# Optimization experiments

Measured on AMD Instinct MI355X. Metric: run time of the kernel, lower is better.

## Reference

```python
import jax, jax.numpy as jnp
import numpy as np

M_TIME = 64      # signal model output length (time points)
N_DICT = 20000   # dictionary entries
B_VOX = 8192     # voxels / batch


def setup_inputs() -> dict:
    key = jax.random.key(0)
    k = jax.random.split(key, 6)
    input_real = jax.random.normal(k[0], (M_TIME, B_VOX), jnp.float32)
    input_imag = jax.random.normal(k[1], (M_TIME, B_VOX), jnp.float32)
    # raw dictionary signals, then normalize columns as append() does
    yr = jax.random.normal(k[2], (M_TIME, N_DICT), jnp.float32)
    yi = jax.random.normal(k[3], (M_TIME, N_DICT), jnp.float32)
    norm = jnp.sqrt(jnp.sum(yr * yr + yi * yi, axis=0))  # (N,)
    inverse_norm_y = 1.0 / norm
    y_real = yr * inverse_norm_y
    y_imag = yi * inverse_norm_y
    x_t1 = jax.random.uniform(k[4], (N_DICT,), jnp.float32, 0.1, 3.0)
    x_t2 = jax.random.uniform(k[5], (N_DICT,), jnp.float32, 0.01, 0.5)
    return {
        'input_real': input_real, 'input_imag': input_imag,
        'y_real': y_real, 'y_imag': y_imag,
        'inverse_norm_y': inverse_norm_y, 'x_t1': x_t1, 'x_t2': x_t2,
    }


def reference(input_real, input_imag, y_real, y_imag, inverse_norm_y, x_t1, x_t2):
    # |<y_n, s_b>|^2 for complex y and complex input, via 4 real GEMMs (as in the
    # original module): sim[n, b]
    sim = (jnp.einsum('mb,mn->nb', input_real, y_real) ** 2
           + jnp.einsum('mb,mn->nb', input_real, y_imag) ** 2
           + jnp.einsum('mb,mn->nb', input_imag, y_real) ** 2
           + jnp.einsum('mb,mn->nb', input_imag, y_imag) ** 2)
    idx = jnp.argmax(sim, axis=0)  # (B,)
    # scale = sum_m conj(y[:, idx]) * input * inverse_norm_y[idx]
    yr = y_real[:, idx]   # (M, B)
    yi = y_imag[:, idx]   # (M, B)
    inv = inverse_norm_y[idx]  # (B,)
    scale_r = jnp.sum(yr * input_real + yi * input_imag, axis=0) * inv
    scale_i = jnp.sum(yr * input_imag - yi * input_real, axis=0) * inv
    # returns (scale, t1, t2) with complex scale split into real/imag, stacked (4, B)
    return jnp.stack([scale_r, scale_i, x_t1[idx], x_t2[idx]])
```

## Files before the change

kernel.cpp:

```cpp
#include <hip/hip_runtime.h>
#include <hip/hip_bf16.h>
#include <stdint.h>

#define M_TIME 64
#define N_DICT 20000
#define B_VOX  8192

#define NTILES 313

typedef _Float16 v8h __attribute__((ext_vector_type(8)));
typedef float    v4f __attribute__((ext_vector_type(4)));
typedef float    v2f __attribute__((ext_vector_type(2)));

__device__ __forceinline__ unsigned long long u64max(unsigned long long a, unsigned long long b) { return a > b ? a : b; }
__device__ __forceinline__ unsigned umin32(unsigned a, unsigned b) { return a < b ? a : b; }
__device__ __forceinline__ unsigned umax32(unsigned a, unsigned b) { return a > b ? a : b; }
__device__ __forceinline__ unsigned umed3(unsigned a, unsigned b, unsigned c) {
    unsigned d;
    asm("v_med3_u32 %0, %1, %2, %3" : "=v"(d) : "v"(a), "v"(b), "v"(c));
    return d;
}

__global__ __launch_bounds__(256) void split_y(
    const float* __restrict__ yr, const float* __restrict__ yi,
    v8h* __restrict__ yp)
{
    const int u = blockIdx.x * 256 + threadIdx.x;
    const int n_l = u & 63;
    const int j   = (u >> 6) & 7;
    const int T   = (u >> 9) % NTILES;
    const int arr = u / (NTILES * 512);
    if (arr > 1) return;
    const float* P = arr ? yi : yr;
    const int n_g = T * 64 + n_l;
    v8h V;
#pragma unroll
    for (int c = 0; c < 8; ++c) {
        float v = 0.f;
        if (n_g < N_DICT) v = P[(j * 8 + c) * N_DICT + n_g];
        V[c] = (_Float16)v;
    }
    const int fr = (arr * 2 + (j >> 2)) * 4 + (j & 3);
    yp[((size_t)T * 16 + fr) * 64 + n_l] = V;
}

__global__ __launch_bounds__(256, 2) void gemm_pre(
    const float* __restrict__ ir, const float* __restrict__ ii,
    const v8h* __restrict__ yp,
    unsigned* __restrict__ cand, int tpc, int slots)
{
    __shared__ unsigned xm[2][2][16][2];

    const int tid  = threadIdx.x;
    const int wave = tid >> 6, lane = tid & 63;
    const int quad = lane >> 4, col = lane & 15;
    const int wb   = wave >> 1, wn = wave & 1;
    const int vox_w = blockIdx.x * 64 + wb * 32;
    const int chunk = blockIdx.y;
    const int T0 = chunk * tpc;
    const int T1 = (T0 + tpc < NTILES) ? T0 + tpc : NTILES;

    v8h fh[2][2][2];
#pragma unroll
    for (int arr = 0; arr < 2; ++arr) {
        const float* P = arr ? ii : ir;
#pragma unroll
        for (int bt = 0; bt < 2; ++bt) {
            const int b = vox_w + bt * 16 + col;
#pragma unroll
            for (int h = 0; h < 2; ++h) {
                v8h H;
#pragma unroll
                for (int j = 0; j < 8; ++j) {
                    const int k = h * 32 + quad * 8 + j;
                    H[j] = (_Float16)P[k * B_VOX + b];
                }
                fh[arr][bt][h] = H;
            }
        }
    }

    v8h yfr[2][2], yfi[2][2];
    auto loadf = [&](int T) {
        const v8h* yv = (const v8h*)((const char*)yp + (size_t)T * 16384);
#pragma unroll
        for (int h = 0; h < 2; ++h)
#pragma unroll
            for (int nt = 0; nt < 2; ++nt) {
                const int nrow = (wn * 2 + nt) * 16 + col;
                yfr[h][nt] = yv[((0 * 2 + h) * 4 + quad) * 64 + nrow];
                yfi[h][nt] = yv[((1 * 2 + h) * 4 + quad) * 64 + nrow];
            }
    };

    const v4f zc = {0.f, 0.f, 0.f, 0.f};
    unsigned t2a[2] = {0u, 0u}, t2b[2] = {0u, 0u};

    loadf(T0);
    for (int T = T0; T < T1; ++T) {
        v4f acc[2][2][4];
#pragma unroll
        for (int h = 0; h < 2; ++h) {
#pragma unroll
            for (int nt = 0; nt < 2; ++nt) {
#pragma unroll
                for (int bt = 0; bt < 2; ++bt) {
#define MF(A, B, C) __builtin_amdgcn_mfma_f32_16x16x32_f16(A, B, C, 0, 0, 0)
                    if (h == 0) {
                        acc[bt][nt][0] = MF(yfr[0][nt], fh[0][bt][0], zc);
                        acc[bt][nt][1] = MF(yfi[0][nt], fh[0][bt][0], zc);
                        acc[bt][nt][2] = MF(yfr[0][nt], fh[1][bt][0], zc);
                        acc[bt][nt][3] = MF(yfi[0][nt], fh[1][bt][0], zc);
                    } else {
                        acc[bt][nt][0] = MF(yfr[1][nt], fh[0][bt][1], acc[bt][nt][0]);
                        acc[bt][nt][1] = MF(yfi[1][nt], fh[0][bt][1], acc[bt][nt][1]);
                        acc[bt][nt][2] = MF(yfr[1][nt], fh[1][bt][1], acc[bt][nt][2]);
                        acc[bt][nt][3] = MF(yfi[1][nt], fh[1][bt][1], acc[bt][nt][3]);
                    }
#undef MF
                }
            }
        }

        if (T + 1 < T1) loadf(T + 1);

        const int tl = T - T0;
#pragma unroll
        for (int nt = 0; nt < 2; ++nt) {
            const unsigned base = 0x1FFFu
                - (unsigned)(tl * 64 + (wn * 2 + nt) * 16 + quad * 4);
            v2f s01[2], s23[2];
#pragma unroll
            for (int bt = 0; bt < 2; ++bt) {
                const v4f a0 = acc[bt][nt][0], a1 = acc[bt][nt][1];
                const v4f a2 = acc[bt][nt][2], a3 = acc[bt][nt][3];
                {
                    const v2f p0 = __builtin_shufflevector(a0, a0, 0, 1);
                    const v2f p1 = __builtin_shufflevector(a1, a1, 0, 1);
                    const v2f p2 = __builtin_shufflevector(a2, a2, 0, 1);
                    const v2f p3 = __builtin_shufflevector(a3, a3, 0, 1);
                    v2f s = p0 * p0;
                    s = __builtin_elementwise_fma(p1, p1, s);
                    s = __builtin_elementwise_fma(p2, p2, s);
                    s = __builtin_elementwise_fma(p3, p3, s);
                    s01[bt] = s;
                }
                {
                    const v2f p0 = __builtin_shufflevector(a0, a0, 2, 3);
                    const v2f p1 = __builtin_shufflevector(a1, a1, 2, 3);
                    const v2f p2 = __builtin_shufflevector(a2, a2, 2, 3);
                    const v2f p3 = __builtin_shufflevector(a3, a3, 2, 3);
                    v2f s = p0 * p0;
                    s = __builtin_elementwise_fma(p1, p1, s);
                    s = __builtin_elementwise_fma(p2, p2, s);
                    s = __builtin_elementwise_fma(p3, p3, s);
                    s23[bt] = s;
                }
            }
#pragma unroll
            for (int r = 0; r < 4; ++r) {
#pragma unroll
                for (int bt = 0; bt < 2; ++bt) {
                    const float s = (r < 2) ? s01[bt][r] : s23[bt][r - 2];
                    const unsigned pb = (__float_as_uint(s) & 0xFFFFE000u)
                                      | (base - (unsigned)r);
                    const unsigned nb = umed3(pb, t2a[bt], t2b[bt]);
                    t2a[bt] = umax32(pb, t2a[bt]);
                    t2b[bt] = nb;
                }
            }
        }
    }

    unsigned fa1[2], fa2[2];
#pragma unroll
    for (int bt = 0; bt < 2; ++bt) {
        unsigned a1 = t2a[bt], a2 = t2b[bt];
#pragma unroll
        for (int d = 16; d <= 32; d <<= 1) {
            unsigned b1 = (unsigned)__shfl_xor((int)a1, d, 64);
            unsigned b2 = (unsigned)__shfl_xor((int)a2, d, 64);
            unsigned mn = umin32(a1, b1);
            a1 = umax32(a1, b1);
            a2 = umax32(mn, umax32(a2, b2));
        }
        fa1[bt] = a1; fa2[bt] = a2;
    }
    __syncthreads();
    if (wn == 1 && lane < 16) {
#pragma unroll
        for (int bt = 0; bt < 2; ++bt) { xm[wb][bt][lane][0] = fa1[bt]; xm[wb][bt][lane][1] = fa2[bt]; }
    }
    __syncthreads();
    if (wn == 0 && lane < 16) {
#pragma unroll
        for (int bt = 0; bt < 2; ++bt) {
            unsigned b1 = xm[wb][bt][lane][0];
            unsigned b2 = xm[wb][bt][lane][1];
            unsigned m1 = umax32(fa1[bt], b1);
            unsigned m2 = umax32(umin32(fa1[bt], b1), umax32(fa2[bt], b2));
            const size_t vox = vox_w + bt * 16 + lane;
            cand[vox * slots + chunk * 2 + 0] = m1;
            cand[vox * slots + chunk * 2 + 1] = m2;
        }
    }
}

__global__ __launch_bounds__(256) void rescore_finish(
    const float* __restrict__ ir, const float* __restrict__ ii,
    const float* __restrict__ yr, const float* __restrict__ yi,
    const float* __restrict__ inv, const float* __restrict__ x1,
    const float* __restrict__ x2,
    const unsigned* __restrict__ cand, int slots, int tpc,
    float* __restrict__ out)
{
    const int tid  = threadIdx.x;
    const int vox  = blockIdx.x * 4 + (tid >> 6);
    const int slot = tid & 63;

    unsigned p = (slot < slots) ? cand[(size_t)vox * slots + slot] : 0u;
    float sa = __uint_as_float(p & 0xFFFFE000u);
    const int chunkc = slot >> 1;
    const int nn = chunkc * tpc * 64 + (0x1FFF - (int)(p & 0x1FFFu));

    float amax = sa;
#pragma unroll
    for (int d = 1; d <= 32; d <<= 1) amax = fmaxf(amax, __shfl_xor(amax, d, 64));

    unsigned long long q = 0ull;
    float rr = 0.f, ri = 0.f, s1 = 0.f, s2 = 0.f;
    const bool active = (slot < slots) && (nn >= 0) && (nn < N_DICT)
                     && (sa >= 0.97f * amax);
    if (active) {
        for (int m = 0; m < M_TIME; ++m) {
            float a  = yr[(size_t)m * N_DICT + nn];
            float c  = yi[(size_t)m * N_DICT + nn];
            float vr = ir[m * B_VOX + vox];
            float vi = ii[m * B_VOX + vox];
            rr = fmaf(vr, a, rr); ri = fmaf(vr, c, ri);
            s1 = fmaf(vi, a, s1); s2 = fmaf(vi, c, s2);
        }
        float s = fmaf(rr, rr, fmaf(ri, ri, fmaf(s1, s1, s2 * s2)));
        q = (((unsigned long long)__float_as_uint(s)) << 32)
          | (unsigned long long)(0xFFFFFFFFu - (unsigned)nn);
    }
    unsigned long long qm = q;
#pragma unroll
    for (int d = 1; d <= 32; d <<= 1) qm = u64max(qm, __shfl_xor(qm, d, 64));

    if (active && q == qm && qm != 0ull) {
        float ss = inv[nn];
        out[0 * B_VOX + vox] = (rr + s2) * ss;
        out[1 * B_VOX + vox] = (s1 - ri) * ss;
        out[2 * B_VOX + vox] = x1[nn];
        out[3 * B_VOX + vox] = x2[nn];
    }
}

__global__ __launch_bounds__(256, 3) void argmax_naive(
    const float* __restrict__ ir, const float* __restrict__ ii,
    const float* __restrict__ yr, const float* __restrict__ yi,
    int* __restrict__ idxout)
{
    int b = blockIdx.x * 256 + threadIdx.x;
    float bs = -1.0f; int bn = 0;
    for (int n = 0; n < N_DICT; ++n) {
        float a_rr = 0.f, a_ri = 0.f, a_s1 = 0.f, a_s2 = 0.f;
        for (int m = 0; m < M_TIME; ++m) {
            float a = yr[m * N_DICT + n], c = yi[m * N_DICT + n];
            float vr = ir[m * B_VOX + b], vi = ii[m * B_VOX + b];
            a_rr = fmaf(vr, a, a_rr); a_ri = fmaf(vr, c, a_ri);
            a_s1 = fmaf(vi, a, a_s1); a_s2 = fmaf(vi, c, a_s2);
        }
        float sim = fmaf(a_rr, a_rr, fmaf(a_ri, a_ri, fmaf(a_s1, a_s1, a_s2 * a_s2)));
        if (sim > bs) { bs = sim; bn = n; }
    }
    idxout[b] = bn;
}

__global__ void finish_k(const float* __restrict__ ir, const float* __restrict__ ii,
                         const float* __restrict__ yr, const float* __restrict__ yi,
                         const float* __restrict__ inv, const float* __restrict__ x1,
                         const float* __restrict__ x2,
                         const int* __restrict__ idxin, float* __restrict__ out)
{
    int b = blockIdx.x * blockDim.x + threadIdx.x;
    int idx = idxin[b];
    float ar = 0.f, ai = 0.f;
    for (int m = 0; m < M_TIME; ++m) {
        float a  = yr[(size_t)m * N_DICT + idx];
        float c  = yi[(size_t)m * N_DICT + idx];
        float vr = ir[m * B_VOX + b];
        float vi = ii[m * B_VOX + b];
        ar = fmaf(a, vr, ar); ar = fmaf(c, vi, ar);
        ai = fmaf(a, vi, ai); ai = fmaf(-c, vr, ai);
    }
    float s = inv[idx];
    out[0 * B_VOX + b] = ar * s;
    out[1 * B_VOX + b] = ai * s;
    out[2 * B_VOX + b] = x1[idx];
    out[3 * B_VOX + b] = x2[idx];
}

extern "C" void kernel_launch(void* const* d_in, const int* in_sizes, int n_in,
                              void* d_out, int out_size, void* d_ws, size_t ws_size,
                              hipStream_t stream) {
    const float* ir  = (const float*)d_in[0];
    const float* ii  = (const float*)d_in[1];
    const float* yr  = (const float*)d_in[2];
    const float* yi  = (const float*)d_in[3];
    const float* inv = (const float*)d_in[4];
    const float* x1  = (const float*)d_in[5];
    const float* x2  = (const float*)d_in[6];
    float* out = (float*)d_out;

    const size_t yp_bytes = (size_t)NTILES * 16384;

    int CH = 0;
    for (int c = 32; c >= 4; c >>= 1) {
        size_t cand_bytes = (size_t)B_VOX * (2 * c) * sizeof(unsigned);
        if (ws_size >= cand_bytes + yp_bytes) { CH = c; break; }
    }

    if (CH > 0) {
        const int slots = 2 * CH;
        const int tpc   = (NTILES + CH - 1) / CH;
        unsigned* cand = (unsigned*)d_ws;
        v8h* yp = (v8h*)((char*)d_ws + (size_t)B_VOX * slots * sizeof(unsigned));

        const int units = 2 * NTILES * 512;
        split_y<<<(units + 255) / 256, 256, 0, stream>>>(yr, yi, yp);
        gemm_pre<<<dim3(B_VOX / 64, CH), 256, 0, stream>>>(ir, ii, yp, cand, tpc, slots);
        rescore_finish<<<B_VOX / 4, 256, 0, stream>>>(ir, ii, yr, yi, inv, x1, x2,
                                                      cand, slots, tpc, out);
    } else {
        int* idxo = (int*)(out + 3 * B_VOX);
        argmax_naive<<<B_VOX / 256, 256, 0, stream>>>(ir, ii, yr, yi, idxo);
        finish_k<<<B_VOX / 256, 256, 0, stream>>>(ir, ii, yr, yi,
                                                  inv, x1, x2, idxo, out);
    }
}
```

Before: 188.1 us.

## Repartition GEMM waves so each wave covers all 64 voxels and one dictionary subtile

Each wave used to cover 32 voxels and two 16-row dictionary subtiles. Now each wave owns one 16-row dictionary subtile across all 64 voxels of the block. This halves the per-wave dictionary fragment loads per tile and doubles the voxel fragments kept in registers. The cross-wave top-2 merge now combines four waves through shared memory with a single barrier. The larger input-fragment register footprint could hurt occupancy under the launch bound of 2 blocks per unit.

```diff
diff --git a/kernel.cpp b/kernel.cpp
--- a/kernel.cpp
+++ b/kernel.cpp
@@ -49,23 +49,22 @@
     const v8h* __restrict__ yp,
     unsigned* __restrict__ cand, int tpc, int slots)
 {
-    __shared__ unsigned xm[2][2][16][2];
+    __shared__ unsigned xm[4][4][16][2];
 
     const int tid  = threadIdx.x;
     const int wave = tid >> 6, lane = tid & 63;
     const int quad = lane >> 4, col = lane & 15;
-    const int wb   = wave >> 1, wn = wave & 1;
-    const int vox_w = blockIdx.x * 64 + wb * 32;
+    const int vox_w = blockIdx.x * 64;
     const int chunk = blockIdx.y;
     const int T0 = chunk * tpc;
     const int T1 = (T0 + tpc < NTILES) ? T0 + tpc : NTILES;
 
-    v8h fh[2][2][2];
+    v8h fh[2][4][2];
 #pragma unroll
     for (int arr = 0; arr < 2; ++arr) {
         const float* P = arr ? ii : ir;
 #pragma unroll
-        for (int bt = 0; bt < 2; ++bt) {
+        for (int bt = 0; bt < 4; ++bt) {
             const int b = vox_w + bt * 16 + col;
 #pragma unroll
             for (int h = 0; h < 2; ++h) {
@@ -80,101 +79,84 @@
         }
     }
 
-    v8h yfr[2][2], yfi[2][2];
+    v8h yf[2][2];
     auto loadf = [&](int T) {
         const v8h* yv = (const v8h*)((const char*)yp + (size_t)T * 16384);
-#pragma unroll
-        for (int h = 0; h < 2; ++h)
-#pragma unroll
-            for (int nt = 0; nt < 2; ++nt) {
-                const int nrow = (wn * 2 + nt) * 16 + col;
-                yfr[h][nt] = yv[((0 * 2 + h) * 4 + quad) * 64 + nrow];
-                yfi[h][nt] = yv[((1 * 2 + h) * 4 + quad) * 64 + nrow];
-            }
+        const int nrow = wave * 16 + col;
+#pragma unroll
+        for (int ri = 0; ri < 2; ++ri)
+#pragma unroll
+            for (int h = 0; h < 2; ++h)
+                yf[ri][h] = yv[((ri * 2 + h) * 4 + quad) * 64 + nrow];
     };
 
     const v4f zc = {0.f, 0.f, 0.f, 0.f};
-    unsigned t2a[2] = {0u, 0u}, t2b[2] = {0u, 0u};
+    unsigned t2a[4] = {0u, 0u, 0u, 0u}, t2b[4] = {0u, 0u, 0u, 0u};
 
     loadf(T0);
     for (int T = T0; T < T1; ++T) {
-        v4f acc[2][2][4];
-#pragma unroll
-        for (int h = 0; h < 2; ++h) {
-#pragma unroll
-            for (int nt = 0; nt < 2; ++nt) {
-#pragma unroll
-                for (int bt = 0; bt < 2; ++bt) {
+        const int tl = T - T0;
+        v4f acc[4][4];
 #define MF(A, B, C) __builtin_amdgcn_mfma_f32_16x16x32_f16(A, B, C, 0, 0, 0)
-                    if (h == 0) {
-                        acc[bt][nt][0] = MF(yfr[0][nt], fh[0][bt][0], zc);
-                        acc[bt][nt][1] = MF(yfi[0][nt], fh[0][bt][0], zc);
-                        acc[bt][nt][2] = MF(yfr[0][nt], fh[1][bt][0], zc);
-                        acc[bt][nt][3] = MF(yfi[0][nt], fh[1][bt][0], zc);
-                    } else {
-                        acc[bt][nt][0] = MF(yfr[1][nt], fh[0][bt][1], acc[bt][nt][0]);
-                        acc[bt][nt][1] = MF(yfi[1][nt], fh[0][bt][1], acc[bt][nt][1]);
-                        acc[bt][nt][2] = MF(yfr[1][nt], fh[1][bt][1], acc[bt][nt][2]);
-                        acc[bt][nt][3] = MF(yfi[1][nt], fh[1][bt][1], acc[bt][nt][3]);
-                    }
+#pragma unroll
+        for (int bt = 0; bt < 4; ++bt) {
+            acc[bt][0] = MF(yf[0][0], fh[0][bt][0], zc);
+            acc[bt][1] = MF(yf[1][0], fh[0][bt][0], zc);
+            acc[bt][2] = MF(yf[0][0], fh[1][bt][0], zc);
+            acc[bt][3] = MF(yf[1][0], fh[1][bt][0], zc);
+        }
+#pragma unroll
+        for (int bt = 0; bt < 4; ++bt) {
+            acc[bt][0] = MF(yf[0][1], fh[0][bt][1], acc[bt][0]);
+            acc[bt][1] = MF(yf[1][1], fh[0][bt][1], acc[bt][1]);
+            acc[bt][2] = MF(yf[0][1], fh[1][bt][1], acc[bt][2]);
+            acc[bt][3] = MF(yf[1][1], fh[1][bt][1], acc[bt][3]);
+        }
 #undef MF
-                }
-            }
-        }
-
         if (T + 1 < T1) loadf(T + 1);
 
-        const int tl = T - T0;
-#pragma unroll
-        for (int nt = 0; nt < 2; ++nt) {
-            const unsigned base = 0x1FFFu
-                - (unsigned)(tl * 64 + (wn * 2 + nt) * 16 + quad * 4);
-            v2f s01[2], s23[2];
-#pragma unroll
-            for (int bt = 0; bt < 2; ++bt) {
-                const v4f a0 = acc[bt][nt][0], a1 = acc[bt][nt][1];
-                const v4f a2 = acc[bt][nt][2], a3 = acc[bt][nt][3];
-                {
-                    const v2f p0 = __builtin_shufflevector(a0, a0, 0, 1);
-                    const v2f p1 = __builtin_shufflevector(a1, a1, 0, 1);
-                    const v2f p2 = __builtin_shufflevector(a2, a2, 0, 1);
-                    const v2f p3 = __builtin_shufflevector(a3, a3, 0, 1);
-                    v2f s = p0 * p0;
-                    s = __builtin_elementwise_fma(p1, p1, s);
-                    s = __builtin_elementwise_fma(p2, p2, s);
-                    s = __builtin_elementwise_fma(p3, p3, s);
-                    s01[bt] = s;
-                }
-                {
-                    const v2f p0 = __builtin_shufflevector(a0, a0, 2, 3);
-                    const v2f p1 = __builtin_shufflevector(a1, a1, 2, 3);
-                    const v2f p2 = __builtin_shufflevector(a2, a2, 2, 3);
-                    const v2f p3 = __builtin_shufflevector(a3, a3, 2, 3);
-                    v2f s = p0 * p0;
-                    s = __builtin_elementwise_fma(p1, p1, s);
-                    s = __builtin_elementwise_fma(p2, p2, s);
-                    s = __builtin_elementwise_fma(p3, p3, s);
-                    s23[bt] = s;
-                }
+        const unsigned base = 0x1FFFu
+            - (unsigned)(tl * 64 + wave * 16 + quad * 4);
+#pragma unroll
+        for (int bt = 0; bt < 4; ++bt) {
+            v2f s01, s23;
+            {
+                const v2f p0 = __builtin_shufflevector(acc[bt][0], acc[bt][0], 0, 1);
+                const v2f p1 = __builtin_shufflevector(acc[bt][1], acc[bt][1], 0, 1);
+                const v2f p2 = __builtin_shufflevector(acc[bt][2], acc[bt][2], 0, 1);
+                const v2f p3 = __builtin_shufflevector(acc[bt][3], acc[bt][3], 0, 1);
+                v2f s = p0 * p0;
+                s = __builtin_elementwise_fma(p1, p1, s);
+                s = __builtin_elementwise_fma(p2, p2, s);
+                s = __builtin_elementwise_fma(p3, p3, s);
+                s01 = s;
+            }
+            {
+                const v2f p0 = __builtin_shufflevector(acc[bt][0], acc[bt][0], 2, 3);
+                const v2f p1 = __builtin_shufflevector(acc[bt][1], acc[bt][1], 2, 3);
+                const v2f p2 = __builtin_shufflevector(acc[bt][2], acc[bt][2], 2, 3);
+                const v2f p3 = __builtin_shufflevector(acc[bt][3], acc[bt][3], 2, 3);
+                v2f s = p0 * p0;
+                s = __builtin_elementwise_fma(p1, p1, s);
+                s = __builtin_elementwise_fma(p2, p2, s);
+                s = __builtin_elementwise_fma(p3, p3, s);
+                s23 = s;
             }
 #pragma unroll
             for (int r = 0; r < 4; ++r) {
-#pragma unroll
-                for (int bt = 0; bt < 2; ++bt) {
-                    const float s = (r < 2) ? s01[bt][r] : s23[bt][r - 2];
-                    const unsigned pb = (__float_as_uint(s) & 0xFFFFE000u)
-                                      | (base - (unsigned)r);
-                    const unsigned nb = umed3(pb, t2a[bt], t2b[bt]);
-                    t2a[bt] = umax32(pb, t2a[bt]);
-                    t2b[bt] = nb;
-                }
-            }
-        }
-    }
-
-    unsigned fa1[2], fa2[2];
-#pragma unroll
-    for (int bt = 0; bt < 2; ++bt) {
+                const float s = (r < 2) ? s01[r] : s23[r - 2];
+                const unsigned pb = (__float_as_uint(s) & 0xFFFFE000u)
+                                  | (base - (unsigned)r);
+                const unsigned nb = umed3(pb, t2a[bt], t2b[bt]);
+                t2a[bt] = umax32(pb, t2a[bt]);
+                t2b[bt] = nb;
+            }
+        }
+    }
+
+    unsigned fa1[4], fa2[4];
+#pragma unroll
+    for (int bt = 0; bt < 4; ++bt) {
         unsigned a1 = t2a[bt], a2 = t2b[bt];
 #pragma unroll
         for (int d = 16; d <= 32; d <<= 1) {
@@ -186,19 +168,25 @@
         }
         fa1[bt] = a1; fa2[bt] = a2;
     }
+    if (lane < 16) {
+#pragma unroll
+        for (int bt = 0; bt < 4; ++bt) {
+            xm[wave][bt][lane][0] = fa1[bt];
+            xm[wave][bt][lane][1] = fa2[bt];
+        }
+    }
     __syncthreads();
-    if (wn == 1 && lane < 16) {
-#pragma unroll
-        for (int bt = 0; bt < 2; ++bt) { xm[wb][bt][lane][0] = fa1[bt]; xm[wb][bt][lane][1] = fa2[bt]; }
-    }
-    __syncthreads();
-    if (wn == 0 && lane < 16) {
-#pragma unroll
-        for (int bt = 0; bt < 2; ++bt) {
-            unsigned b1 = xm[wb][bt][lane][0];
-            unsigned b2 = xm[wb][bt][lane][1];
-            unsigned m1 = umax32(fa1[bt], b1);
-            unsigned m2 = umax32(umin32(fa1[bt], b1), umax32(fa2[bt], b2));
+    if (wave == 0 && lane < 16) {
+#pragma unroll
+        for (int bt = 0; bt < 4; ++bt) {
+            unsigned m1 = 0u, m2 = 0u;
+#pragma unroll
+            for (int w = 0; w < 4; ++w) {
+                const unsigned b1 = xm[w][bt][lane][0];
+                const unsigned b2 = xm[w][bt][lane][1];
+                m2 = umax32(m2, umax32(b2, umin32(m1, b1)));
+                m1 = umax32(m1, b1);
+            }
             const size_t vox = vox_w + bt * 16 + lane;
             cand[vox * slots + chunk * 2 + 0] = m1;
             cand[vox * slots + chunk * 2 + 1] = m2;
```

After: 186.2 us, median of 2. No clear change (-1.0%).
